# Kernel optimization log

Measured on AMD Instinct MI355X. Metric: run time of the kernel, lower is better.

Reference implementation:

```python
import jax, jax.numpy as jnp
import numpy as np

B, T, D, H = 64, 512, 300, 1024
EPS = 1e-5


def setup_inputs() -> dict:
    key = jax.random.key(0)
    ks = jax.random.split(key, 9)
    x = jax.random.normal(ks[0], (B, T, D), jnp.float32)
    t = jax.random.bernoulli(ks[1], 0.5, (B,)).astype(jnp.float32)
    # LockedDropout mask: Bernoulli(1-0.5) / (1-0.5), fixed across timesteps
    mask = jax.random.bernoulli(ks[2], 0.5, (B, H)).astype(jnp.float32) / 0.5
    s = 1.0 / np.sqrt(H)
    W_ih = jax.random.uniform(ks[3], (4 * H, D), jnp.float32, -s, s)
    W_hh = jax.random.uniform(ks[4], (4 * H, H), jnp.float32, -s, s)
    b_ih = jax.random.uniform(ks[5], (4 * H,), jnp.float32, -s, s)
    b_hh = jax.random.uniform(ks[6], (4 * H,), jnp.float32, -s, s)
    gamma = jnp.ones((H,), jnp.float32)
    beta = jnp.zeros((H,), jnp.float32)
    sf = 1.0 / np.sqrt(H)
    fc_w = jax.random.uniform(ks[7], (1, H), jnp.float32, -sf, sf)
    fc_b = jax.random.uniform(ks[8], (1,), jnp.float32, -sf, sf)
    return {"x": x, "t": t, "mask": mask, "W_ih": W_ih, "W_hh": W_hh,
            "b_ih": b_ih, "b_hh": b_hh, "gamma": gamma, "beta": beta,
            "fc_w": fc_w, "fc_b": fc_b}


def reference(x, t, mask, W_ih, W_hh, b_ih, b_hh, gamma, beta, fc_w, fc_b):
    Bs, Ts, _ = x.shape
    Hs = W_hh.shape[1]

    def step(carry, xt):  # xt: [B, D]
        h, c = carry
        gates = xt @ W_ih.T + b_ih + h @ W_hh.T + b_hh  # [B, 4H]
        i, f, g, o = jnp.split(gates, 4, axis=1)        # torch LSTMCell gate order
        c2 = jax.nn.sigmoid(f) * c + jax.nn.sigmoid(i) * jnp.tanh(g)
        h2 = jax.nn.sigmoid(o) * jnp.tanh(c2)           # raw LSTM state carried forward
        # BatchNorm1d in train mode: biased batch statistics
        mu = h2.mean(axis=0)
        var = h2.var(axis=0)
        hn = gamma * (h2 - mu) * jax.lax.rsqrt(var + EPS) + beta
        return (h2, c2), hn * mask                      # locked dropout, fixed mask

    h0 = jnp.zeros((Bs, Hs), x.dtype)
    c0 = jnp.zeros((Bs, Hs), x.dtype)
    _, outs = jax.lax.scan(step, (h0, c0), jnp.swapaxes(x, 0, 1))  # outs: [T, B, H]
    pooled = outs.max(axis=0)                            # MaxPool1d over all timesteps
    z = (pooled @ fc_w.T + fc_b)[:, 0]                   # [B] logits
    # BCEWithLogitsLoss (mean reduction), numerically stable
    loss = jnp.mean(jnp.logaddexp(0.0, z) - z * t)
    return (loss, z)
```

## Files before the change

kernel.cpp:

```cpp
#include <hip/hip_runtime.h>
#include <cstddef>
#include <cstdint>

#define BB 64
#define TT 512
#define HH 1024
#define DD 300
#define NTH 256
#define NBLK 128
#define HB 8
#define XPAD 320
#define KS_X 10
#define KS_H 32
#define BN_EPS 1e-5f

typedef short short8 __attribute__((ext_vector_type(8)));
typedef float f32x4 __attribute__((ext_vector_type(4)));
typedef unsigned u32x2 __attribute__((ext_vector_type(2)));

__device__ __forceinline__ float sigmoid_f(float v) {
  v = fminf(fmaxf(v, -30.f), 30.f);
  return 1.f / (1.f + __expf(-v));
}
__device__ __forceinline__ float tanh_f(float v) {
  float e = __expf(fminf(fmaxf(2.f * v, -30.f), 30.f));
  return (e - 1.f) / (e + 1.f);
}
__device__ __forceinline__ unsigned short tobf(float f) {
  unsigned u = __float_as_uint(f);
  u += 0x7fffu + ((u >> 16) & 1u);
  return (unsigned short)(u >> 16);
}

__device__ __forceinline__ void ldA_sc(const void* p, short8& d) {
  asm volatile("global_load_dwordx4 %0, %1, off sc0 sc1"
               : "=v"(d) : "v"(p) : "memory");
}
__device__ __forceinline__ void ldA_nc(const void* p, short8& d) {
  asm volatile("global_load_dwordx4 %0, %1, off"
               : "=v"(d) : "v"(p) : "memory");
}
__device__ __forceinline__ void ld4_sc(const void* p, f32x4& d) {
  asm volatile("global_load_dwordx4 %0, %1, off sc0 sc1"
               : "=v"(d) : "v"(p) : "memory");
}
__device__ __forceinline__ u32x2 ld2w_sc(const void* p) {
  u32x2 v;
  asm volatile("global_load_dwordx2 %0, %1, off sc0 sc1\n\ts_waitcnt vmcnt(0)"
               : "=v"(v) : "v"(p) : "memory");
  return v;
}
__device__ __forceinline__ void st_sc32(void* p, unsigned v) {
  asm volatile("global_store_dword %0, %1, off sc0 sc1\n\ts_waitcnt vmcnt(0)"
               :: "v"(p), "v"(v) : "memory");
}
#define WAITV(N)                                                   \
  do {                                                             \
    asm volatile("s_waitcnt vmcnt(" #N ")" ::: "memory");          \
    __builtin_amdgcn_sched_barrier(0);                             \
  } while (0)

__device__ __forceinline__ f32x4 mfma16(short8 a, short8 b, f32x4 c) {
  return __builtin_amdgcn_mfma_f32_16x16x32_bf16(a, b, c, 0, 0, 0);
}

__device__ __forceinline__ void poll_ge(const unsigned* slots, int tid, unsigned ep) {
  int it = 0;
  for (;;) {
    int ok = 1;
    if (tid < 64) {
      u32x2 v = ld2w_sc(&slots[2 * tid]);
      ok = (v.x >= ep && v.y >= ep) ? 1 : 0;
    }
    if (__syncthreads_and(ok)) break;
    if (++it > (1 << 20)) break;
    if (it > 1) __builtin_amdgcn_s_sleep(1);
  }
}

__global__ void init_k(unsigned* __restrict__ base, int ndw) {
  int idx = blockIdx.x * blockDim.x + threadIdx.x;
  for (int i = idx; i < ndw; i += gridDim.x * blockDim.x) st_sc32(base + i, 0u);
}

__global__ void xcvt_k(const float* __restrict__ x, unsigned short* __restrict__ xbf) {
  const int total = TT * BB * XPAD;
  for (int idx = blockIdx.x * blockDim.x + threadIdx.x; idx < total;
       idx += gridDim.x * blockDim.x) {
    int kx = idx % XPAD;
    int tb = idx / XPAD;
    int b = tb % BB, t = tb / BB;
    float v = (kx < DD) ? x[(size_t)b * (TT * DD) + (size_t)t * DD + kx] : 0.f;
    xbf[idx] = tobf(v);
  }
}

__global__ void __launch_bounds__(NTH, 1)
lstm_mfma(const float* __restrict__ Wih, const float* __restrict__ Whh,
          const float* __restrict__ bih, const float* __restrict__ bhh,
          const float* __restrict__ gammap, const float* __restrict__ betap,
          const float* __restrict__ maskp, const float* __restrict__ tlbl,
          const float* __restrict__ fcw, const float* __restrict__ fcb,
          const unsigned short* __restrict__ xbf, unsigned short* __restrict__ hbuf,
          float* __restrict__ partial, unsigned* __restrict__ slots,
          float* __restrict__ outp) {
  __shared__ short8 Wlds[2][KS_H + KS_X][64];
  __shared__ float Cs[64][33];
  __shared__ float red_s[4][64];

  const int tid = threadIdx.x;
  const int w = tid >> 6, l = tid & 63;
  const int blk = blockIdx.x;
  const int hb0 = blk * HB;

  for (int idx = tid; idx < 2 * (KS_H + KS_X) * 64; idx += NTH) {
    int nt = idx / ((KS_H + KS_X) * 64);
    int rem = idx % ((KS_H + KS_X) * 64);
    int ks = rem >> 6, ll = rem & 63;
    int colq = nt * 16 + (ll & 15);
    int g = colq >> 3, j = colq & 7;
    int r = g * HH + hb0 + j;
    int k0 = (ll >> 4) * 8;
    float v[8];
    if (ks < KS_H) {
      const float* src = Whh + (size_t)r * HH + ks * 32 + k0;
      f32x4 u0 = *(const f32x4*)src;
      f32x4 u1 = *(const f32x4*)(src + 4);
      v[0] = u0.x; v[1] = u0.y; v[2] = u0.z; v[3] = u0.w;
      v[4] = u1.x; v[5] = u1.y; v[6] = u1.z; v[7] = u1.w;
    } else {
      int d0 = (ks - KS_H) * 32 + k0;
#pragma unroll
      for (int e = 0; e < 8; ++e)
        v[e] = (d0 + e < DD) ? Wih[(size_t)r * DD + d0 + e] : 0.f;
    }
    short8 pk;
#pragma unroll
    for (int e = 0; e < 8; ++e) pk[e] = (short)tobf(v[e]);
    Wlds[nt][ks][ll] = pk;
  }

  const int row = w * 16 + (l & 15);
  const int lk16 = (l >> 4);

  const int b = l, j0 = 2 * w, j1 = 2 * w + 1;
  const float gam0 = gammap[hb0 + j0], gam1 = gammap[hb0 + j1];
  const float bet0 = betap[hb0 + j0], bet1 = betap[hb0 + j1];
  const float msk0 = maskp[(size_t)b * HH + hb0 + j0];
  const float msk1 = maskp[(size_t)b * HH + hb0 + j1];
  const float biI0 = bih[0 * HH + hb0 + j0] + bhh[0 * HH + hb0 + j0];
  const float biF0 = bih[1 * HH + hb0 + j0] + bhh[1 * HH + hb0 + j0];
  const float biG0 = bih[2 * HH + hb0 + j0] + bhh[2 * HH + hb0 + j0];
  const float biO0 = bih[3 * HH + hb0 + j0] + bhh[3 * HH + hb0 + j0];
  const float biI1 = bih[0 * HH + hb0 + j1] + bhh[0 * HH + hb0 + j1];
  const float biF1 = bih[1 * HH + hb0 + j1] + bhh[1 * HH + hb0 + j1];
  const float biG1 = bih[2 * HH + hb0 + j1] + bhh[2 * HH + hb0 + j1];
  const float biO1 = bih[3 * HH + hb0 + j1] + bhh[3 * HH + hb0 + j1];
  const float fw0 = fcw[hb0 + j0], fw1 = fcw[hb0 + j1];
  float creg0 = 0.f, creg1 = 0.f;
  float pool0 = -3.4e38f, pool1 = -3.4e38f;
  __syncthreads();

  for (int s = 0; s < TT; ++s) {
    const unsigned short* hc = hbuf + (size_t)(s & 1) * (BB * HH);
    unsigned short* hnx = hbuf + (size_t)((s + 1) & 1) * (BB * HH);

    const unsigned short* px = xbf + ((size_t)s * BB + row) * XPAD + lk16 * 8;
    short8 xa[KS_X];
#pragma unroll
    for (int i = 0; i < KS_X; ++i) ldA_nc(px + i * 32, xa[i]);
    WAITV(0);
    f32x4 acc0 = {0.f, 0.f, 0.f, 0.f}, acc1 = {0.f, 0.f, 0.f, 0.f};
#pragma unroll
    for (int i = 0; i < KS_X; ++i) {
      acc0 = mfma16(xa[i], Wlds[0][KS_H + i][l], acc0);
      acc1 = mfma16(xa[i], Wlds[1][KS_H + i][l], acc1);
    }

    poll_ge(slots, tid, (unsigned)s);

    const unsigned short* ph = hc + (size_t)lk16 * 512 + row * 8;
    short8 ha[KS_H];
#pragma unroll
    for (int i = 0; i < 8; ++i) ldA_sc(ph + i * 2048, ha[i]);
#pragma unroll
    for (int i = 8; i < 16; ++i) ldA_sc(ph + i * 2048, ha[i]);
    WAITV(8);
#pragma unroll
    for (int i = 16; i < 24; ++i) ldA_sc(ph + i * 2048, ha[i]);
#pragma unroll
    for (int i = 0; i < 8; ++i) {
      acc0 = mfma16(ha[i], Wlds[0][i][l], acc0);
      acc1 = mfma16(ha[i], Wlds[1][i][l], acc1);
    }
    WAITV(8);
#pragma unroll
    for (int i = 24; i < 32; ++i) ldA_sc(ph + i * 2048, ha[i]);
#pragma unroll
    for (int i = 8; i < 16; ++i) {
      acc0 = mfma16(ha[i], Wlds[0][i][l], acc0);
      acc1 = mfma16(ha[i], Wlds[1][i][l], acc1);
    }
    WAITV(8);
#pragma unroll
    for (int i = 16; i < 24; ++i) {
      acc0 = mfma16(ha[i], Wlds[0][i][l], acc0);
      acc1 = mfma16(ha[i], Wlds[1][i][l], acc1);
    }
    WAITV(0);
#pragma unroll
    for (int i = 24; i < 32; ++i) {
      acc0 = mfma16(ha[i], Wlds[0][i][l], acc0);
      acc1 = mfma16(ha[i], Wlds[1][i][l], acc1);
    }

    {
      int crow = w * 16 + (l >> 4) * 4;
      int cc0 = (l & 15), cc1 = 16 + (l & 15);
#pragma unroll
      for (int r = 0; r < 4; ++r) {
        Cs[crow + r][cc0] = acc0[r];
        Cs[crow + r][cc1] = acc1[r];
      }
    }
    __syncthreads();

    float gI0 = Cs[b][j0] + biI0, gF0 = Cs[b][8 + j0] + biF0;
    float gG0 = Cs[b][16 + j0] + biG0, gO0 = Cs[b][24 + j0] + biO0;
    float gI1 = Cs[b][j1] + biI1, gF1 = Cs[b][8 + j1] + biF1;
    float gG1 = Cs[b][16 + j1] + biG1, gO1 = Cs[b][24 + j1] + biO1;
    float c20 = sigmoid_f(gF0) * creg0 + sigmoid_f(gI0) * tanh_f(gG0);
    float h20 = sigmoid_f(gO0) * tanh_f(c20);
    float c21 = sigmoid_f(gF1) * creg1 + sigmoid_f(gI1) * tanh_f(gG1);
    float h21 = sigmoid_f(gO1) * tanh_f(c21);
    creg0 = c20;
    creg1 = c21;
    float s10 = h20, s20 = h20 * h20, s11 = h21, s21 = h21 * h21;
#pragma unroll
    for (int off = 32; off; off >>= 1) {
      s10 += __shfl_xor(s10, off, 64);
      s20 += __shfl_xor(s20, off, 64);
      s11 += __shfl_xor(s11, off, 64);
      s21 += __shfl_xor(s21, off, 64);
    }
    float mu0 = s10 * (1.f / 64.f), var0 = fmaf(-mu0, mu0, s20 * (1.f / 64.f));
    float mu1 = s11 * (1.f / 64.f), var1 = fmaf(-mu1, mu1, s21 * (1.f / 64.f));
    float hn0 = gam0 * (h20 - mu0) * rsqrtf(var0 + BN_EPS) + bet0;
    float hn1 = gam1 * (h21 - mu1) * rsqrtf(var1 + BN_EPS) + bet1;
    pool0 = fmaxf(pool0, hn0 * msk0);
    pool1 = fmaxf(pool1, hn1 * msk1);
    unsigned pk = (unsigned)tobf(h20) | ((unsigned)tobf(h21) << 16);
    st_sc32((unsigned*)(hnx + (size_t)blk * 512 + b * 8) + w, pk);
    __syncthreads();
    if (tid == 0) st_sc32(&slots[blk], (unsigned)(s + 1));
  }

  red_s[w][b] = pool0 * fw0 + pool1 * fw1;
  __syncthreads();
  if (tid < BB) {
    float part = red_s[0][tid] + red_s[1][tid] + red_s[2][tid] + red_s[3][tid];
    st_sc32(&partial[(size_t)tid * NBLK + blk], __float_as_uint(part));
  }
  __syncthreads();
  if (tid == 0) st_sc32(&slots[blk], (unsigned)(TT + 1));
  if (blk != 0) return;

  poll_ge(slots, tid, (unsigned)(TT + 1));
  {
    int fb = tid & 63, q = tid >> 6;
    const float* pp = partial + ((size_t)fb * NBLK + q * 32);
    f32x4 v0, v1, v2, v3, v4, v5, v6, v7;
    ld4_sc(pp + 0, v0);  ld4_sc(pp + 4, v1);  ld4_sc(pp + 8, v2);  ld4_sc(pp + 12, v3);
    ld4_sc(pp + 16, v4); ld4_sc(pp + 20, v5); ld4_sc(pp + 24, v6); ld4_sc(pp + 28, v7);
    WAITV(0);
    float sum = v0.x + v0.y + v0.z + v0.w + v1.x + v1.y + v1.z + v1.w +
                v2.x + v2.y + v2.z + v2.w + v3.x + v3.y + v3.z + v3.w +
                v4.x + v4.y + v4.z + v4.w + v5.x + v5.y + v5.z + v5.w +
                v6.x + v6.y + v6.z + v6.w + v7.x + v7.y + v7.z + v7.w;
    red_s[q][fb] = sum;
  }
  __syncthreads();
  if (tid < BB) {
    float z = red_s[0][tid] + red_s[1][tid] + red_s[2][tid] + red_s[3][tid] + fcb[0];
    outp[1 + tid] = z;
    float sp = fmaxf(z, 0.f) + log1pf(__expf(-fabsf(z)));
    float lt = sp - z * tlbl[tid];
#pragma unroll
    for (int off = 32; off; off >>= 1) lt += __shfl_xor(lt, off, 64);
    if (tid == 0) outp[0] = lt * (1.f / 64.f);
  }
}

extern "C" void kernel_launch(void* const* d_in, const int* in_sizes, int n_in,
                              void* d_out, int out_size, void* d_ws, size_t ws_size,
                              hipStream_t stream) {
  const float* x = (const float*)d_in[0];
  const float* tlbl = (const float*)d_in[1];
  const float* maskp = (const float*)d_in[2];
  const float* Wih = (const float*)d_in[3];
  const float* Whh = (const float*)d_in[4];
  const float* bih = (const float*)d_in[5];
  const float* bhh = (const float*)d_in[6];
  const float* gammap = (const float*)d_in[7];
  const float* betap = (const float*)d_in[8];
  const float* fcw = (const float*)d_in[9];
  const float* fcb = (const float*)d_in[10];
  float* outp = (float*)d_out;

  unsigned* slots = (unsigned*)d_ws;
  unsigned short* hbuf = (unsigned short*)((char*)d_ws + 4096);
  float* partial = (float*)((char*)d_ws + 4096 + 2 * BB * HH * 2);
  unsigned short* xbf =
      (unsigned short*)((char*)d_ws + 4096 + 2 * BB * HH * 2 + BB * NBLK * 4);

  int ndw = (4096 + BB * HH * 2) / 4;
  hipLaunchKernelGGL(init_k, dim3(64), dim3(NTH), 0, stream, (unsigned*)d_ws, ndw);
  hipLaunchKernelGGL(xcvt_k, dim3(2048), dim3(NTH), 0, stream, x, xbf);
  hipLaunchKernelGGL(lstm_mfma, dim3(NBLK), dim3(NTH), 0, stream,
                     Wih, Whh, bih, bhh, gammap, betap, maskp, tlbl, fcw, fcb,
                     xbf, hbuf, partial, slots, outp);
}
```

Measured before the change: 2.695 ms.

## Prefetch next-step x, batch h loads, and vectorize state publish per step

```diff
diff --git a/kernel.cpp b/kernel.cpp
--- a/kernel.cpp
+++ b/kernel.cpp
@@ -17,6 +17,7 @@
 typedef short short8 __attribute__((ext_vector_type(8)));
 typedef float f32x4 __attribute__((ext_vector_type(4)));
 typedef unsigned u32x2 __attribute__((ext_vector_type(2)));
+typedef unsigned u32x4 __attribute__((ext_vector_type(4)));
 
 __device__ __forceinline__ float sigmoid_f(float v) {
   v = fminf(fmaxf(v, -30.f), 30.f);
@@ -52,6 +53,14 @@
 }
 __device__ __forceinline__ void st_sc32(void* p, unsigned v) {
   asm volatile("global_store_dword %0, %1, off sc0 sc1\n\ts_waitcnt vmcnt(0)"
+               :: "v"(p), "v"(v) : "memory");
+}
+__device__ __forceinline__ void st_sc32_nd(void* p, unsigned v) {
+  asm volatile("global_store_dword %0, %1, off sc0 sc1"
+               :: "v"(p), "v"(v) : "memory");
+}
+__device__ __forceinline__ void st4_sc_nd(void* p, u32x4 v) {
+  asm volatile("global_store_dwordx4 %0, %1, off sc0 sc1"
                :: "v"(p), "v"(v) : "memory");
 }
 #define WAITV(N)                                                   \
@@ -74,7 +83,7 @@
     }
     if (__syncthreads_and(ok)) break;
     if (++it > (1 << 20)) break;
-    if (it > 1) __builtin_amdgcn_s_sleep(1);
+    if (it > 2) __builtin_amdgcn_s_sleep(1);
   }
 }
 
@@ -106,6 +115,7 @@
           float* __restrict__ outp) {
   __shared__ short8 Wlds[2][KS_H + KS_X][64];
   __shared__ float Cs[64][33];
+  __shared__ unsigned pkbuf[BB][4];
   __shared__ float red_s[4][64];
 
   const int tid = threadIdx.x;
@@ -143,76 +153,84 @@
   const int row = w * 16 + (l & 15);
   const int lk16 = (l >> 4);
 
+  const int cq = l & 15;
+  const float bcol0 = bih[(cq >> 3) * HH + hb0 + (cq & 7)] +
+                      bhh[(cq >> 3) * HH + hb0 + (cq & 7)];
+  const float bcol1 = bih[(2 + (cq >> 3)) * HH + hb0 + (cq & 7)] +
+                      bhh[(2 + (cq >> 3)) * HH + hb0 + (cq & 7)];
+
   const int b = l, j0 = 2 * w, j1 = 2 * w + 1;
   const float gam0 = gammap[hb0 + j0], gam1 = gammap[hb0 + j1];
   const float bet0 = betap[hb0 + j0], bet1 = betap[hb0 + j1];
   const float msk0 = maskp[(size_t)b * HH + hb0 + j0];
   const float msk1 = maskp[(size_t)b * HH + hb0 + j1];
-  const float biI0 = bih[0 * HH + hb0 + j0] + bhh[0 * HH + hb0 + j0];
-  const float biF0 = bih[1 * HH + hb0 + j0] + bhh[1 * HH + hb0 + j0];
-  const float biG0 = bih[2 * HH + hb0 + j0] + bhh[2 * HH + hb0 + j0];
-  const float biO0 = bih[3 * HH + hb0 + j0] + bhh[3 * HH + hb0 + j0];
-  const float biI1 = bih[0 * HH + hb0 + j1] + bhh[0 * HH + hb0 + j1];
-  const float biF1 = bih[1 * HH + hb0 + j1] + bhh[1 * HH + hb0 + j1];
-  const float biG1 = bih[2 * HH + hb0 + j1] + bhh[2 * HH + hb0 + j1];
-  const float biO1 = bih[3 * HH + hb0 + j1] + bhh[3 * HH + hb0 + j1];
   const float fw0 = fcw[hb0 + j0], fw1 = fcw[hb0 + j1];
   float creg0 = 0.f, creg1 = 0.f;
   float pool0 = -3.4e38f, pool1 = -3.4e38f;
+
+  short8 xa[KS_X];
+  {
+    const unsigned short* px = xbf + ((size_t)0 * BB + row) * XPAD + lk16 * 8;
+#pragma unroll
+    for (int i = 0; i < KS_X; ++i) ldA_nc(px + i * 32, xa[i]);
+  }
   __syncthreads();
 
   for (int s = 0; s < TT; ++s) {
     const unsigned short* hc = hbuf + (size_t)(s & 1) * (BB * HH);
     unsigned short* hnx = hbuf + (size_t)((s + 1) & 1) * (BB * HH);
 
-    const unsigned short* px = xbf + ((size_t)s * BB + row) * XPAD + lk16 * 8;
-    short8 xa[KS_X];
-#pragma unroll
-    for (int i = 0; i < KS_X; ++i) ldA_nc(px + i * 32, xa[i]);
-    WAITV(0);
-    f32x4 acc0 = {0.f, 0.f, 0.f, 0.f}, acc1 = {0.f, 0.f, 0.f, 0.f};
-#pragma unroll
-    for (int i = 0; i < KS_X; ++i) {
-      acc0 = mfma16(xa[i], Wlds[0][KS_H + i][l], acc0);
-      acc1 = mfma16(xa[i], Wlds[1][KS_H + i][l], acc1);
-    }
-
     poll_ge(slots, tid, (unsigned)s);
 
     const unsigned short* ph = hc + (size_t)lk16 * 512 + row * 8;
     short8 ha[KS_H];
 #pragma unroll
-    for (int i = 0; i < 8; ++i) ldA_sc(ph + i * 2048, ha[i]);
-#pragma unroll
-    for (int i = 8; i < 16; ++i) ldA_sc(ph + i * 2048, ha[i]);
+    for (int i = 0; i < KS_H; ++i) ldA_sc(ph + i * 2048, ha[i]);
+
+    WAITV(32);
+
+    f32x4 acc0a = {bcol0, bcol0, bcol0, bcol0}, acc0b = {0.f, 0.f, 0.f, 0.f};
+    f32x4 acc1a = {bcol1, bcol1, bcol1, bcol1}, acc1b = {0.f, 0.f, 0.f, 0.f};
+#pragma unroll
+    for (int i = 0; i < KS_X; i += 2) {
+      acc0a = mfma16(xa[i], Wlds[0][KS_H + i][l], acc0a);
+      acc1a = mfma16(xa[i], Wlds[1][KS_H + i][l], acc1a);
+      acc0b = mfma16(xa[i + 1], Wlds[0][KS_H + i + 1][l], acc0b);
+      acc1b = mfma16(xa[i + 1], Wlds[1][KS_H + i + 1][l], acc1b);
+    }
+    WAITV(24);
+#pragma unroll
+    for (int i = 0; i < 8; i += 2) {
+      acc0a = mfma16(ha[i], Wlds[0][i][l], acc0a);
+      acc1a = mfma16(ha[i], Wlds[1][i][l], acc1a);
+      acc0b = mfma16(ha[i + 1], Wlds[0][i + 1][l], acc0b);
+      acc1b = mfma16(ha[i + 1], Wlds[1][i + 1][l], acc1b);
+    }
+    WAITV(16);
+#pragma unroll
+    for (int i = 8; i < 16; i += 2) {
+      acc0a = mfma16(ha[i], Wlds[0][i][l], acc0a);
+      acc1a = mfma16(ha[i], Wlds[1][i][l], acc1a);
+      acc0b = mfma16(ha[i + 1], Wlds[0][i + 1][l], acc0b);
+      acc1b = mfma16(ha[i + 1], Wlds[1][i + 1][l], acc1b);
+    }
     WAITV(8);
 #pragma unroll
-    for (int i = 16; i < 24; ++i) ldA_sc(ph + i * 2048, ha[i]);
-#pragma unroll
-    for (int i = 0; i < 8; ++i) {
-      acc0 = mfma16(ha[i], Wlds[0][i][l], acc0);
-      acc1 = mfma16(ha[i], Wlds[1][i][l], acc1);
-    }
-    WAITV(8);
-#pragma unroll
-    for (int i = 24; i < 32; ++i) ldA_sc(ph + i * 2048, ha[i]);
-#pragma unroll
-    for (int i = 8; i < 16; ++i) {
-      acc0 = mfma16(ha[i], Wlds[0][i][l], acc0);
-      acc1 = mfma16(ha[i], Wlds[1][i][l], acc1);
-    }
-    WAITV(8);
-#pragma unroll
-    for (int i = 16; i < 24; ++i) {
-      acc0 = mfma16(ha[i], Wlds[0][i][l], acc0);
-      acc1 = mfma16(ha[i], Wlds[1][i][l], acc1);
+    for (int i = 16; i < 24; i += 2) {
+      acc0a = mfma16(ha[i], Wlds[0][i][l], acc0a);
+      acc1a = mfma16(ha[i], Wlds[1][i][l], acc1a);
+      acc0b = mfma16(ha[i + 1], Wlds[0][i + 1][l], acc0b);
+      acc1b = mfma16(ha[i + 1], Wlds[1][i + 1][l], acc1b);
     }
     WAITV(0);
 #pragma unroll
-    for (int i = 24; i < 32; ++i) {
-      acc0 = mfma16(ha[i], Wlds[0][i][l], acc0);
-      acc1 = mfma16(ha[i], Wlds[1][i][l], acc1);
-    }
+    for (int i = 24; i < 32; i += 2) {
+      acc0a = mfma16(ha[i], Wlds[0][i][l], acc0a);
+      acc1a = mfma16(ha[i], Wlds[1][i][l], acc1a);
+      acc0b = mfma16(ha[i + 1], Wlds[0][i + 1][l], acc0b);
+      acc1b = mfma16(ha[i + 1], Wlds[1][i + 1][l], acc1b);
+    }
+    f32x4 acc0 = acc0a + acc0b, acc1 = acc1a + acc1b;
 
     {
       int crow = w * 16 + (l >> 4) * 4;
@@ -223,12 +241,18 @@
         Cs[crow + r][cc1] = acc1[r];
       }
     }
+    {
+      int sx = (s + 1 < TT) ? s + 1 : s;
+      const unsigned short* px = xbf + ((size_t)sx * BB + row) * XPAD + lk16 * 8;
+#pragma unroll
+      for (int i = 0; i < KS_X; ++i) ldA_nc(px + i * 32, xa[i]);
+    }
     __syncthreads();
 
-    float gI0 = Cs[b][j0] + biI0, gF0 = Cs[b][8 + j0] + biF0;
-    float gG0 = Cs[b][16 + j0] + biG0, gO0 = Cs[b][24 + j0] + biO0;
-    float gI1 = Cs[b][j1] + biI1, gF1 = Cs[b][8 + j1] + biF1;
-    float gG1 = Cs[b][16 + j1] + biG1, gO1 = Cs[b][24 + j1] + biO1;
+    float gI0 = Cs[b][j0],      gF0 = Cs[b][8 + j0];
+    float gG0 = Cs[b][16 + j0], gO0 = Cs[b][24 + j0];
+    float gI1 = Cs[b][j1],      gF1 = Cs[b][8 + j1];
+    float gG1 = Cs[b][16 + j1], gO1 = Cs[b][24 + j1];
     float c20 = sigmoid_f(gF0) * creg0 + sigmoid_f(gI0) * tanh_f(gG0);
     float h20 = sigmoid_f(gO0) * tanh_f(c20);
     float c21 = sigmoid_f(gF1) * creg1 + sigmoid_f(gI1) * tanh_f(gG1);
@@ -249,10 +273,15 @@
     float hn1 = gam1 * (h21 - mu1) * rsqrtf(var1 + BN_EPS) + bet1;
     pool0 = fmaxf(pool0, hn0 * msk0);
     pool1 = fmaxf(pool1, hn1 * msk1);
-    unsigned pk = (unsigned)tobf(h20) | ((unsigned)tobf(h21) << 16);
-    st_sc32((unsigned*)(hnx + (size_t)blk * 512 + b * 8) + w, pk);
+    pkbuf[b][w] = (unsigned)tobf(h20) | ((unsigned)tobf(h21) << 16);
     __syncthreads();
-    if (tid == 0) st_sc32(&slots[blk], (unsigned)(s + 1));
+
+    if (w == 2) {
+      u32x4 pv = {pkbuf[l][0], pkbuf[l][1], pkbuf[l][2], pkbuf[l][3]};
+      st4_sc_nd(hnx + (size_t)blk * 512 + l * 8, pv);
+      WAITV(0);
+      if (l == 0) st_sc32_nd(&slots[blk], (unsigned)(s + 1));
+    }
   }
 
   red_s[w][b] = pool0 * fw0 + pool1 * fw1;
@@ -262,10 +291,10 @@
     st_sc32(&partial[(size_t)tid * NBLK + blk], __float_as_uint(part));
   }
   __syncthreads();
-  if (tid == 0) st_sc32(&slots[blk], (unsigned)(TT + 1));
+  if (tid == 0) st_sc32_nd(&slots[blk], (unsigned)(TT + 2));
   if (blk != 0) return;
 
-  poll_ge(slots, tid, (unsigned)(TT + 1));
+  poll_ge(slots, tid, (unsigned)(TT + 2));
   {
     int fb = tid & 63, q = tid >> 6;
     const float* pp = partial + ((size_t)fb * NBLK + q * 32);
```

After: 3.134 ms. +16.3%, slower.

## Halve persistent LSTM blocks, stream W_ih fragments from global, widen per-block hidden slice

Applied to the files above, without the earlier changes.

```diff
diff --git a/kernel.cpp b/kernel.cpp
--- a/kernel.cpp
+++ b/kernel.cpp
@@ -7,8 +7,9 @@
 #define HH 1024
 #define DD 300
 #define NTH 256
-#define NBLK 128
-#define HB 8
+#define NBLK 64
+#define HB 16
+#define NTN 4
 #define XPAD 320
 #define KS_X 10
 #define KS_H 32
@@ -44,14 +45,22 @@
   asm volatile("global_load_dwordx4 %0, %1, off sc0 sc1"
                : "=v"(d) : "v"(p) : "memory");
 }
-__device__ __forceinline__ u32x2 ld2w_sc(const void* p) {
-  u32x2 v;
-  asm volatile("global_load_dwordx2 %0, %1, off sc0 sc1\n\ts_waitcnt vmcnt(0)"
+__device__ __forceinline__ unsigned ld_sc(const void* p) {
+  unsigned v;
+  asm volatile("global_load_dword %0, %1, off sc0 sc1\n\ts_waitcnt vmcnt(0)"
                : "=v"(v) : "v"(p) : "memory");
   return v;
 }
 __device__ __forceinline__ void st_sc32(void* p, unsigned v) {
   asm volatile("global_store_dword %0, %1, off sc0 sc1\n\ts_waitcnt vmcnt(0)"
+               :: "v"(p), "v"(v) : "memory");
+}
+__device__ __forceinline__ void st_sc32_nd(void* p, unsigned v) {
+  asm volatile("global_store_dword %0, %1, off sc0 sc1"
+               :: "v"(p), "v"(v) : "memory");
+}
+__device__ __forceinline__ void st2_sc(void* p, u32x2 v) {
+  asm volatile("global_store_dwordx2 %0, %1, off sc0 sc1\n\ts_waitcnt vmcnt(0)"
                :: "v"(p), "v"(v) : "memory");
 }
 #define WAITV(N)                                                   \
@@ -68,13 +77,10 @@
   int it = 0;
   for (;;) {
     int ok = 1;
-    if (tid < 64) {
-      u32x2 v = ld2w_sc(&slots[2 * tid]);
-      ok = (v.x >= ep && v.y >= ep) ? 1 : 0;
-    }
+    if (tid < 64) ok = (ld_sc(&slots[tid]) >= ep) ? 1 : 0;
     if (__syncthreads_and(ok)) break;
     if (++it > (1 << 20)) break;
-    if (it > 1) __builtin_amdgcn_s_sleep(1);
+    if (it > 2) __builtin_amdgcn_s_sleep(1);
   }
 }
 
@@ -95,17 +101,37 @@
   }
 }
 
+__global__ void wihfrag_k(const float* __restrict__ Wih,
+                          unsigned short* __restrict__ wfr) {
+  int idx = blockIdx.x * blockDim.x + threadIdx.x;
+  const int total = NBLK * KS_X * NTN * 64;
+  for (; idx < total; idx += gridDim.x * blockDim.x) {
+    int ll = idx & 63;
+    int rest = idx >> 6;
+    int nt = rest & 3;
+    rest >>= 2;
+    int ks = rest % KS_X, bk = rest / KS_X;
+    int r = nt * HH + bk * HB + (ll & 15);
+    int k0 = ks * 32 + (ll >> 4) * 8;
+    short8 pk;
+#pragma unroll
+    for (int e = 0; e < 8; ++e)
+      pk[e] = (k0 + e < DD) ? (short)tobf(Wih[(size_t)r * DD + k0 + e]) : (short)0;
+    *(short8*)(wfr + (size_t)idx * 8) = pk;
+  }
+}
+
 __global__ void __launch_bounds__(NTH, 1)
-lstm_mfma(const float* __restrict__ Wih, const float* __restrict__ Whh,
-          const float* __restrict__ bih, const float* __restrict__ bhh,
-          const float* __restrict__ gammap, const float* __restrict__ betap,
-          const float* __restrict__ maskp, const float* __restrict__ tlbl,
-          const float* __restrict__ fcw, const float* __restrict__ fcb,
-          const unsigned short* __restrict__ xbf, unsigned short* __restrict__ hbuf,
-          float* __restrict__ partial, unsigned* __restrict__ slots,
-          float* __restrict__ outp) {
-  __shared__ short8 Wlds[2][KS_H + KS_X][64];
-  __shared__ float Cs[64][33];
+lstm_mfma(const float* __restrict__ Whh, const float* __restrict__ bih,
+          const float* __restrict__ bhh, const float* __restrict__ gammap,
+          const float* __restrict__ betap, const float* __restrict__ maskp,
+          const float* __restrict__ tlbl, const float* __restrict__ fcw,
+          const float* __restrict__ fcb, const unsigned short* __restrict__ xbf,
+          const unsigned short* __restrict__ wfrag,
+          unsigned short* __restrict__ hbuf, float* __restrict__ partial,
+          unsigned* __restrict__ slots, float* __restrict__ outp) {
+  __shared__ short8 Wlds[NTN][KS_H][64];
+  __shared__ float Cs[64][65];
   __shared__ float red_s[4][64];
 
   const int tid = threadIdx.x;
@@ -113,171 +139,192 @@
   const int blk = blockIdx.x;
   const int hb0 = blk * HB;
 
-  for (int idx = tid; idx < 2 * (KS_H + KS_X) * 64; idx += NTH) {
-    int nt = idx / ((KS_H + KS_X) * 64);
-    int rem = idx % ((KS_H + KS_X) * 64);
+  for (int idx = tid; idx < NTN * KS_H * 64; idx += NTH) {
+    int nt = idx / (KS_H * 64);
+    int rem = idx % (KS_H * 64);
     int ks = rem >> 6, ll = rem & 63;
-    int colq = nt * 16 + (ll & 15);
-    int g = colq >> 3, j = colq & 7;
-    int r = g * HH + hb0 + j;
-    int k0 = (ll >> 4) * 8;
-    float v[8];
-    if (ks < KS_H) {
-      const float* src = Whh + (size_t)r * HH + ks * 32 + k0;
-      f32x4 u0 = *(const f32x4*)src;
-      f32x4 u1 = *(const f32x4*)(src + 4);
-      v[0] = u0.x; v[1] = u0.y; v[2] = u0.z; v[3] = u0.w;
-      v[4] = u1.x; v[5] = u1.y; v[6] = u1.z; v[7] = u1.w;
-    } else {
-      int d0 = (ks - KS_H) * 32 + k0;
+    int r = nt * HH + hb0 + (ll & 15);
+    int k0 = ks * 32 + (ll >> 4) * 8;
+    const float* src = Whh + (size_t)r * HH + k0;
+    f32x4 u0 = *(const f32x4*)src;
+    f32x4 u1 = *(const f32x4*)(src + 4);
+    short8 pk;
+    pk[0] = (short)tobf(u0.x); pk[1] = (short)tobf(u0.y);
+    pk[2] = (short)tobf(u0.z); pk[3] = (short)tobf(u0.w);
+    pk[4] = (short)tobf(u1.x); pk[5] = (short)tobf(u1.y);
+    pk[6] = (short)tobf(u1.z); pk[7] = (short)tobf(u1.w);
+    Wlds[nt][ks][ll] = pk;
+  }
+
+  const int row = w * 16 + (l & 15);
+  const int lk16 = l >> 4;
+
+  float bcol[NTN];
 #pragma unroll
-      for (int e = 0; e < 8; ++e)
-        v[e] = (d0 + e < DD) ? Wih[(size_t)r * DD + d0 + e] : 0.f;
-    }
-    short8 pk;
+  for (int nt = 0; nt < NTN; ++nt)
+    bcol[nt] = bih[nt * HH + hb0 + (l & 15)] + bhh[nt * HH + hb0 + (l & 15)];
+
+  const int b = l;
+  float gam[4], bet[4], msk[4], fw[4], creg[4], pool[4];
 #pragma unroll
-    for (int e = 0; e < 8; ++e) pk[e] = (short)tobf(v[e]);
-    Wlds[nt][ks][ll] = pk;
-  }
-
-  const int row = w * 16 + (l & 15);
-  const int lk16 = (l >> 4);
-
-  const int b = l, j0 = 2 * w, j1 = 2 * w + 1;
-  const float gam0 = gammap[hb0 + j0], gam1 = gammap[hb0 + j1];
-  const float bet0 = betap[hb0 + j0], bet1 = betap[hb0 + j1];
-  const float msk0 = maskp[(size_t)b * HH + hb0 + j0];
-  const float msk1 = maskp[(size_t)b * HH + hb0 + j1];
-  const float biI0 = bih[0 * HH + hb0 + j0] + bhh[0 * HH + hb0 + j0];
-  const float biF0 = bih[1 * HH + hb0 + j0] + bhh[1 * HH + hb0 + j0];
-  const float biG0 = bih[2 * HH + hb0 + j0] + bhh[2 * HH + hb0 + j0];
-  const float biO0 = bih[3 * HH + hb0 + j0] + bhh[3 * HH + hb0 + j0];
-  const float biI1 = bih[0 * HH + hb0 + j1] + bhh[0 * HH + hb0 + j1];
-  const float biF1 = bih[1 * HH + hb0 + j1] + bhh[1 * HH + hb0 + j1];
-  const float biG1 = bih[2 * HH + hb0 + j1] + bhh[2 * HH + hb0 + j1];
-  const float biO1 = bih[3 * HH + hb0 + j1] + bhh[3 * HH + hb0 + j1];
-  const float fw0 = fcw[hb0 + j0], fw1 = fcw[hb0 + j1];
-  float creg0 = 0.f, creg1 = 0.f;
-  float pool0 = -3.4e38f, pool1 = -3.4e38f;
+  for (int i = 0; i < 4; ++i) {
+    int j = 4 * w + i;
+    gam[i] = gammap[hb0 + j];
+    bet[i] = betap[hb0 + j];
+    msk[i] = maskp[(size_t)b * HH + hb0 + j];
+    fw[i] = fcw[hb0 + j];
+    creg[i] = 0.f;
+    pool[i] = -3.4e38f;
+  }
+
+  const unsigned short* wfb = wfrag + (size_t)blk * (KS_X * NTN * 64 * 8);
   __syncthreads();
 
   for (int s = 0; s < TT; ++s) {
     const unsigned short* hc = hbuf + (size_t)(s & 1) * (BB * HH);
     unsigned short* hnx = hbuf + (size_t)((s + 1) & 1) * (BB * HH);
 
-    const unsigned short* px = xbf + ((size_t)s * BB + row) * XPAD + lk16 * 8;
-    short8 xa[KS_X];
-#pragma unroll
-    for (int i = 0; i < KS_X; ++i) ldA_nc(px + i * 32, xa[i]);
+    poll_ge(slots, tid, (unsigned)s);
+
+    const unsigned short* phb =
+        hc + (size_t)(lk16 >> 1) * 1024 + row * 16 + (lk16 & 1) * 8;
+    short8 ha[KS_H], xa[KS_X], xb[20];
+
+    #pragma unroll
+    for (int i = 0; i < 8; ++i) ldA_sc(phb + i * 2048, ha[i]);
+    #pragma unroll
+    for (int i = 8; i < 16; ++i) ldA_sc(phb + i * 2048, ha[i]);
+    {
+      const unsigned short* px = xbf + ((size_t)s * BB + row) * XPAD + lk16 * 8;
+      #pragma unroll
+      for (int i = 0; i < KS_X; ++i) ldA_nc(px + i * 32, xa[i]);
+    }
+    #pragma unroll
+    for (int ks = 0; ks < 5; ++ks)
+      #pragma unroll
+      for (int nt = 0; nt < NTN; ++nt)
+        ldA_nc(wfb + ((ks * NTN + nt) * 64 + l) * 8, xb[ks * 4 + nt]);
+
+    f32x4 acc[NTN];
+    #pragma unroll
+    for (int nt = 0; nt < NTN; ++nt)
+      acc[nt] = (f32x4){bcol[nt], bcol[nt], bcol[nt], bcol[nt]};
+
+    WAITV(38);
+    #pragma unroll
+    for (int i = 0; i < 8; ++i)
+      #pragma unroll
+      for (int nt = 0; nt < NTN; ++nt)
+        acc[nt] = mfma16(ha[i], Wlds[nt][i][l], acc[nt]);
+    WAITV(30);
+    #pragma unroll
+    for (int i = 8; i < 16; ++i)
+      #pragma unroll
+      for (int nt = 0; nt < NTN; ++nt)
+        acc[nt] = mfma16(ha[i], Wlds[nt][i][l], acc[nt]);
+    #pragma unroll
+    for (int i = 16; i < 24; ++i) ldA_sc(phb + i * 2048, ha[i]);
+    WAITV(8);
+    #pragma unroll
+    for (int ks = 0; ks < 5; ++ks)
+      #pragma unroll
+      for (int nt = 0; nt < NTN; ++nt)
+        acc[nt] = mfma16(xa[ks], xb[ks * 4 + nt], acc[nt]);
+    #pragma unroll
+    for (int ks = 5; ks < 10; ++ks)
+      #pragma unroll
+      for (int nt = 0; nt < NTN; ++nt)
+        ldA_nc(wfb + ((ks * NTN + nt) * 64 + l) * 8, xb[(ks - 5) * 4 + nt]);
+    WAITV(20);
+    #pragma unroll
+    for (int i = 16; i < 24; ++i)
+      #pragma unroll
+      for (int nt = 0; nt < NTN; ++nt)
+        acc[nt] = mfma16(ha[i], Wlds[nt][i][l], acc[nt]);
+    #pragma unroll
+    for (int i = 24; i < 32; ++i) ldA_sc(phb + i * 2048, ha[i]);
+    WAITV(8);
+    #pragma unroll
+    for (int ks = 5; ks < 10; ++ks)
+      #pragma unroll
+      for (int nt = 0; nt < NTN; ++nt)
+        acc[nt] = mfma16(xa[ks], xb[(ks - 5) * 4 + nt], acc[nt]);
     WAITV(0);
-    f32x4 acc0 = {0.f, 0.f, 0.f, 0.f}, acc1 = {0.f, 0.f, 0.f, 0.f};
-#pragma unroll
-    for (int i = 0; i < KS_X; ++i) {
-      acc0 = mfma16(xa[i], Wlds[0][KS_H + i][l], acc0);
-      acc1 = mfma16(xa[i], Wlds[1][KS_H + i][l], acc1);
-    }
-
-    poll_ge(slots, tid, (unsigned)s);
-
-    const unsigned short* ph = hc + (size_t)lk16 * 512 + row * 8;
-    short8 ha[KS_H];
-#pragma unroll
-    for (int i = 0; i < 8; ++i) ldA_sc(ph + i * 2048, ha[i]);
-#pragma unroll
-    for (int i = 8; i < 16; ++i) ldA_sc(ph + i * 2048, ha[i]);
-    WAITV(8);
-#pragma unroll
-    for (int i = 16; i < 24; ++i) ldA_sc(ph + i * 2048, ha[i]);
-#pragma unroll
-    for (int i = 0; i < 8; ++i) {
-      acc0 = mfma16(ha[i], Wlds[0][i][l], acc0);
-      acc1 = mfma16(ha[i], Wlds[1][i][l], acc1);
-    }
-    WAITV(8);
-#pragma unroll
-    for (int i = 24; i < 32; ++i) ldA_sc(ph + i * 2048, ha[i]);
-#pragma unroll
-    for (int i = 8; i < 16; ++i) {
-      acc0 = mfma16(ha[i], Wlds[0][i][l], acc0);
-      acc1 = mfma16(ha[i], Wlds[1][i][l], acc1);
-    }
-    WAITV(8);
-#pragma unroll
-    for (int i = 16; i < 24; ++i) {
-      acc0 = mfma16(ha[i], Wlds[0][i][l], acc0);
-      acc1 = mfma16(ha[i], Wlds[1][i][l], acc1);
-    }
-    WAITV(0);
-#pragma unroll
-    for (int i = 24; i < 32; ++i) {
-      acc0 = mfma16(ha[i], Wlds[0][i][l], acc0);
-      acc1 = mfma16(ha[i], Wlds[1][i][l], acc1);
-    }
+    #pragma unroll
+    for (int i = 24; i < 32; ++i)
+      #pragma unroll
+      for (int nt = 0; nt < NTN; ++nt)
+        acc[nt] = mfma16(ha[i], Wlds[nt][i][l], acc[nt]);
 
     {
       int crow = w * 16 + (l >> 4) * 4;
-      int cc0 = (l & 15), cc1 = 16 + (l & 15);
-#pragma unroll
-      for (int r = 0; r < 4; ++r) {
-        Cs[crow + r][cc0] = acc0[r];
-        Cs[crow + r][cc1] = acc1[r];
-      }
+      int cc = l & 15;
+      #pragma unroll
+      for (int nt = 0; nt < NTN; ++nt)
+        #pragma unroll
+        for (int r = 0; r < 4; ++r) Cs[crow + r][nt * 16 + cc] = acc[nt][r];
     }
     __syncthreads();
 
-    float gI0 = Cs[b][j0] + biI0, gF0 = Cs[b][8 + j0] + biF0;
-    float gG0 = Cs[b][16 + j0] + biG0, gO0 = Cs[b][24 + j0] + biO0;
-    float gI1 = Cs[b][j1] + biI1, gF1 = Cs[b][8 + j1] + biF1;
-    float gG1 = Cs[b][16 + j1] + biG1, gO1 = Cs[b][24 + j1] + biO1;
-    float c20 = sigmoid_f(gF0) * creg0 + sigmoid_f(gI0) * tanh_f(gG0);
-    float h20 = sigmoid_f(gO0) * tanh_f(c20);
-    float c21 = sigmoid_f(gF1) * creg1 + sigmoid_f(gI1) * tanh_f(gG1);
-    float h21 = sigmoid_f(gO1) * tanh_f(c21);
-    creg0 = c20;
-    creg1 = c21;
-    float s10 = h20, s20 = h20 * h20, s11 = h21, s21 = h21 * h21;
-#pragma unroll
-    for (int off = 32; off; off >>= 1) {
-      s10 += __shfl_xor(s10, off, 64);
-      s20 += __shfl_xor(s20, off, 64);
-      s11 += __shfl_xor(s11, off, 64);
-      s21 += __shfl_xor(s21, off, 64);
+    float h2[4], s1[4], s2[4];
+    #pragma unroll
+    for (int i = 0; i < 4; ++i) {
+      int j = 4 * w + i;
+      float gI = Cs[b][j], gF = Cs[b][16 + j];
+      float gG = Cs[b][32 + j], gO = Cs[b][48 + j];
+      float c2 = sigmoid_f(gF) * creg[i] + sigmoid_f(gI) * tanh_f(gG);
+      h2[i] = sigmoid_f(gO) * tanh_f(c2);
+      creg[i] = c2;
+      s1[i] = h2[i];
+      s2[i] = h2[i] * h2[i];
     }
-    float mu0 = s10 * (1.f / 64.f), var0 = fmaf(-mu0, mu0, s20 * (1.f / 64.f));
-    float mu1 = s11 * (1.f / 64.f), var1 = fmaf(-mu1, mu1, s21 * (1.f / 64.f));
-    float hn0 = gam0 * (h20 - mu0) * rsqrtf(var0 + BN_EPS) + bet0;
-    float hn1 = gam1 * (h21 - mu1) * rsqrtf(var1 + BN_EPS) + bet1;
-    pool0 = fmaxf(pool0, hn0 * msk0);
-    pool1 = fmaxf(pool1, hn1 * msk1);
-    unsigned pk = (unsigned)tobf(h20) | ((unsigned)tobf(h21) << 16);
-    st_sc32((unsigned*)(hnx + (size_t)blk * 512 + b * 8) + w, pk);
+    #pragma unroll
+    for (int off = 32; off; off >>= 1)
+      #pragma unroll
+      for (int i = 0; i < 4; ++i) {
+        s1[i] += __shfl_xor(s1[i], off, 64);
+        s2[i] += __shfl_xor(s2[i], off, 64);
+      }
+    unsigned pk01, pk23;
+    {
+      float hn[4];
+      #pragma unroll
+      for (int i = 0; i < 4; ++i) {
+        float mu = s1[i] * (1.f / 64.f);
+        float var = fmaf(-mu, mu, s2[i] * (1.f / 64.f));
+        hn[i] = gam[i] * (h2[i] - mu) * rsqrtf(var + BN_EPS) + bet[i];
+        pool[i] = fmaxf(pool[i], hn[i] * msk[i]);
+      }
+      pk01 = (unsigned)tobf(h2[0]) | ((unsigned)tobf(h2[1]) << 16);
+      pk23 = (unsigned)tobf(h2[2]) | ((unsigned)tobf(h2[3]) << 16);
+    }
+    u32x2 pv = {pk01, pk23};
+    st2_sc(hnx + (size_t)blk * 1024 + b * 16 + w * 4, pv);
     __syncthreads();
-    if (tid == 0) st_sc32(&slots[blk], (unsigned)(s + 1));
-  }
-
-  red_s[w][b] = pool0 * fw0 + pool1 * fw1;
+    if (tid == 0) st_sc32_nd(&slots[blk], (unsigned)(s + 1));
+  }
+
+  red_s[w][b] = pool[0] * fw[0] + pool[1] * fw[1] + pool[2] * fw[2] +
+                pool[3] * fw[3];
   __syncthreads();
   if (tid < BB) {
     float part = red_s[0][tid] + red_s[1][tid] + red_s[2][tid] + red_s[3][tid];
     st_sc32(&partial[(size_t)tid * NBLK + blk], __float_as_uint(part));
   }
   __syncthreads();
-  if (tid == 0) st_sc32(&slots[blk], (unsigned)(TT + 1));
+  if (tid == 0) st_sc32_nd(&slots[blk], (unsigned)(TT + 2));
   if (blk != 0) return;
 
-  poll_ge(slots, tid, (unsigned)(TT + 1));
+  poll_ge(slots, tid, (unsigned)(TT + 2));
   {
     int fb = tid & 63, q = tid >> 6;
-    const float* pp = partial + ((size_t)fb * NBLK + q * 32);
-    f32x4 v0, v1, v2, v3, v4, v5, v6, v7;
-    ld4_sc(pp + 0, v0);  ld4_sc(pp + 4, v1);  ld4_sc(pp + 8, v2);  ld4_sc(pp + 12, v3);
-    ld4_sc(pp + 16, v4); ld4_sc(pp + 20, v5); ld4_sc(pp + 24, v6); ld4_sc(pp + 28, v7);
+    const float* pp = partial + ((size_t)fb * NBLK + q * 16);
+    f32x4 v0, v1, v2, v3;
+    ld4_sc(pp + 0, v0); ld4_sc(pp + 4, v1);
+    ld4_sc(pp + 8, v2); ld4_sc(pp + 12, v3);
     WAITV(0);
-    float sum = v0.x + v0.y + v0.z + v0.w + v1.x + v1.y + v1.z + v1.w +
-                v2.x + v2.y + v2.z + v2.w + v3.x + v3.y + v3.z + v3.w +
-                v4.x + v4.y + v4.z + v4.w + v5.x + v5.y + v5.z + v5.w +
-                v6.x + v6.y + v6.z + v6.w + v7.x + v7.y + v7.z + v7.w;
-    red_s[q][fb] = sum;
+    red_s[q][fb] = v0.x + v0.y + v0.z + v0.w + v1.x + v1.y + v1.z + v1.w +
+                   v2.x + v2.y + v2.z + v2.w + v3.x + v3.y + v3.z + v3.w;
   }
   __syncthreads();
   if (tid < BB) {
@@ -310,13 +357,15 @@
   unsigned* slots = (unsigned*)d_ws;
   unsigned short* hbuf = (unsigned short*)((char*)d_ws + 4096);
   float* partial = (float*)((char*)d_ws + 4096 + 2 * BB * HH * 2);
-  unsigned short* xbf =
+  unsigned short* wfrag =
       (unsigned short*)((char*)d_ws + 4096 + 2 * BB * HH * 2 + BB * NBLK * 4);
+  unsigned short* xbf = wfrag + (size_t)NBLK * KS_X * NTN * 64 * 8;
 
   int ndw = (4096 + BB * HH * 2) / 4;
   hipLaunchKernelGGL(init_k, dim3(64), dim3(NTH), 0, stream, (unsigned*)d_ws, ndw);
   hipLaunchKernelGGL(xcvt_k, dim3(2048), dim3(NTH), 0, stream, x, xbf);
+  hipLaunchKernelGGL(wihfrag_k, dim3(640), dim3(NTH), 0, stream, Wih, wfrag);
   hipLaunchKernelGGL(lstm_mfma, dim3(NBLK), dim3(NTH), 0, stream,
-                     Wih, Whh, bih, bhh, gammap, betap, maskp, tlbl, fcw, fcb,
-                     xbf, hbuf, partial, slots, outp);
-}
+                     Whh, bih, bhh, gammap, betap, maskp, tlbl, fcw, fcb,
+                     xbf, wfrag, hbuf, partial, slots, outp);
+}
```

Result: slower. 5.622 ms (+108.6%).
